# Performance work log

Measured on AMD Instinct MI355X. Metric: run time of the kernel, lower is better.

Reference implementation:

```python
import jax, jax.numpy as jnp
import numpy as np

N, IN_SIZE, FEAT, N_OUT = 8192, 512, 128, 512
ALPHA = 0.5


def setup_inputs() -> dict:
    key = jax.random.key(0)
    ks = jax.random.split(key, 5)
    return {
        "x": jax.random.normal(ks[0], (N, IN_SIZE), dtype=jnp.float32),
        "W0": jax.random.normal(ks[1], (FEAT, IN_SIZE), dtype=jnp.float32) * (1.0 / np.sqrt(IN_SIZE)),
        "W1": jax.random.normal(ks[2], (FEAT, IN_SIZE), dtype=jnp.float32) * (1.0 / np.sqrt(IN_SIZE)),
        "weight": jax.random.normal(ks[3], (IN_SIZE, N_OUT), dtype=jnp.float32),
        "weight_time": jax.random.normal(ks[4], (IN_SIZE, N_OUT), dtype=jnp.float32),
    }


def time_affinity(n: int) -> jnp.ndarray:
    # Closed form of the numpy roll/triu/flip construction: M[i,j] = n - |i-j|,
    # then rows normalized to sum to 1.
    idx = jnp.arange(n)
    M = (n - jnp.abs(idx[:, None] - idx[None, :])).astype(jnp.float32)
    return M / jnp.sum(M, axis=1, keepdims=True)


def reference(x, W0, W1, weight, weight_time):
    n = x.shape[0]
    q = x @ W0.T                      # [N, FEAT]
    k = x @ W1.T                      # [N, FEAT]
    G = jax.nn.softmax(q @ k.T, axis=1)   # [N, N] learned affinity
    G_time = time_affinity(n)              # [N, N] static affinity
    out = (G @ x) @ weight                 # [N, N_OUT]
    out_time = (G_time @ x) @ weight_time  # [N, N_OUT]
    return ALPHA * out + (1.0 - ALPHA) * out_time
```

## Files before the change

### kernel.cpp

```cpp
#include <hip/hip_runtime.h>
#include <math.h>

#define NN 8192
#define INS 512
#define FEAT 128

typedef unsigned short ush;
typedef short bf16x8 __attribute__((ext_vector_type(8)));
typedef float f32x4 __attribute__((ext_vector_type(4)));

__device__ __forceinline__ ush f2bf(float f) {
    unsigned u = __float_as_uint(f);
    unsigned r = (u + 0x7FFFu + ((u >> 16) & 1u)) >> 16;
    return (ush)r;
}
__device__ __forceinline__ float bf2f(ush h) {
    return __uint_as_float(((unsigned)h) << 16);
}
__device__ __forceinline__ void cp16(const ush* g, ush* l) {
    __builtin_amdgcn_global_load_lds(
        (const __attribute__((address_space(1))) void*)g,
        (__attribute__((address_space(3))) void*)l, 16, 0, 0);
}
__device__ __forceinline__ void split8(float4 f0, float4 f1, uint4& h, uint4& l) {
    float f[8] = {f0.x, f0.y, f0.z, f0.w, f1.x, f1.y, f1.z, f1.w};
    unsigned hu[8], lu[8];
    #pragma unroll
    for (int j = 0; j < 8; ++j) {
        unsigned u = __float_as_uint(f[j]);
        hu[j] = u >> 16;
        float lo = f[j] - __uint_as_float(u & 0xFFFF0000u);
        lu[j] = (unsigned)f2bf(lo);
    }
    h.x = hu[0] | (hu[1] << 16); h.y = hu[2] | (hu[3] << 16);
    h.z = hu[4] | (hu[5] << 16); h.w = hu[6] | (hu[7] << 16);
    l.x = lu[0] | (lu[1] << 16); l.y = lu[2] | (lu[3] << 16);
    l.z = lu[4] | (lu[5] << 16); l.w = lu[6] | (lu[7] << 16);
}


__global__ __launch_bounds__(256) void cast_w01(const float* __restrict__ W0,
                                                const float* __restrict__ W1,
                                                ush* __restrict__ W01h,
                                                ush* __restrict__ W01l) {
    int idx = (blockIdx.x * 256 + threadIdx.x) * 8;
    int r = idx >> 9, c = idx & 511;
    const float* src = (r < 128) ? &W0[r * 512 + c] : &W1[(r - 128) * 512 + c];
    float4 f0 = *(const float4*)src;
    float4 f1 = *(const float4*)(src + 4);
    uint4 h, l;
    split8(f0, f1, h, l);
    *(uint4*)&W01h[idx] = h;
    *(uint4*)&W01l[idx] = l;
}

__global__ __launch_bounds__(256) void cast_wT(const float* __restrict__ wm,
                                               const float* __restrict__ wt,
                                               ush* __restrict__ wmTh, ush* __restrict__ wmTl,
                                               ush* __restrict__ wtTh, ush* __restrict__ wtTl) {
    const float* src = blockIdx.z ? wt : wm;
    ush* oh = blockIdx.z ? wtTh : wmTh;
    ush* ol = blockIdx.z ? wtTl : wmTl;
    __shared__ float T[64][65];
    const int t = threadIdx.x;
    const int k0 = blockIdx.y * 64, n0 = blockIdx.x * 64;
    #pragma unroll
    for (int u = 0; u < 4; ++u) {
        int idx = u * 256 + t;
        int r = idx >> 4, c4 = (idx & 15) * 4;
        *(float4*)&T[r][c4] = *(const float4*)&src[(k0 + r) * 512 + n0 + c4];
    }
    __syncthreads();
    #pragma unroll
    for (int u = 0; u < 4; ++u) {
        int idx = u * 256 + t;
        int a = idx >> 4, b4 = (idx & 15) * 4;
        unsigned hu[4], lu[4];
        #pragma unroll
        for (int j = 0; j < 4; ++j) {
            float f = T[b4 + j][a];
            unsigned uu = __float_as_uint(f);
            hu[j] = uu >> 16;
            lu[j] = (unsigned)f2bf(f - __uint_as_float(uu & 0xFFFF0000u));
        }
        uint2 hp, lp;
        hp.x = hu[0] | (hu[1] << 16); hp.y = hu[2] | (hu[3] << 16);
        lp.x = lu[0] | (lu[1] << 16); lp.y = lu[2] | (lu[3] << 16);
        *(uint2*)&oh[(n0 + a) * 512 + k0 + b4] = hp;
        *(uint2*)&ol[(n0 + a) * 512 + k0 + b4] = lp;
    }
}

__global__ __launch_bounds__(256, 2) void gemm_xv(const float* __restrict__ x,
    const ush* __restrict__ wmTh, const ush* __restrict__ wmTl,
    const ush* __restrict__ wtTh, const ush* __restrict__ wtTl,
    ush* __restrict__ vtg, ush* __restrict__ xtb) {
    __shared__ __align__(16) ush smA[10240];
    __shared__ __align__(16) ush Bmh[2048], Bml[2048], Bth[2048], Btl[2048];
    ush* Ah = smA;
    ush* Al = smA + 5120;
    const int t = threadIdx.x;
    const int lane = t & 63, w = t >> 6;
    const int l15 = lane & 15, g4 = lane >> 4;
    const int m0 = blockIdx.y * 128, n0 = blockIdx.x * 64;
    const int wm0 = (w & 1) * 64, wn0 = (w >> 1) * 32;
    f32x4 accm[4][2], acct[4][2];
    #pragma unroll
    for (int mt = 0; mt < 4; ++mt)
        #pragma unroll
        for (int nt = 0; nt < 2; ++nt) {
            accm[mt][nt] = (f32x4){0.f, 0.f, 0.f, 0.f};
            acct[mt][nt] = (f32x4){0.f, 0.f, 0.f, 0.f};
        }

    const int am = t >> 1, akh = (t & 1) * 16;
    const int bn = t >> 2, bg = (t & 3) ^ ((t >> 2) & 3);
    for (int k0 = 0; k0 < 512; k0 += 32) {
        __syncthreads();
        {
            const float* src = &x[(m0 + am) * 512 + k0 + akh];
            float4 f0 = *(const float4*)&src[0];
            float4 f1 = *(const float4*)&src[4];
            float4 f2 = *(const float4*)&src[8];
            float4 f3 = *(const float4*)&src[12];
            uint4 h0, l0, h1, l1;
            split8(f0, f1, h0, l0);
            split8(f2, f3, h1, l1);
            int s0 = am * 5 + (akh >> 3);
            *(uint4*)&Ah[s0 * 8] = h0; *(uint4*)&Ah[(s0 + 1) * 8] = h1;
            *(uint4*)&Al[s0 * 8] = l0; *(uint4*)&Al[(s0 + 1) * 8] = l1;
        }
        {
            int srco = (n0 + bn) * 512 + k0 + bg * 8;
            cp16(&wmTh[srco], &Bmh[t * 8]);
            cp16(&wmTl[srco], &Bml[t * 8]);
            cp16(&wtTh[srco], &Bth[t * 8]);
            cp16(&wtTl[srco], &Btl[t * 8]);
        }
        __syncthreads();
        bf16x8 ah[4], al[4];
        #pragma unroll
        for (int mt = 0; mt < 4; ++mt) {
            int slot = (wm0 + mt * 16 + l15) * 5 + g4;
            ah[mt] = *(const bf16x8*)&Ah[slot * 8];
            al[mt] = *(const bf16x8*)&Al[slot * 8];
        }
        bf16x8 bmh[2], bml[2], bth[2], btl[2];
        #pragma unroll
        for (int nt = 0; nt < 2; ++nt) {
            int n = wn0 + nt * 16 + l15;
            int slot = n * 4 + (g4 ^ (n & 3));
            bmh[nt] = *(const bf16x8*)&Bmh[slot * 8];
            bml[nt] = *(const bf16x8*)&Bml[slot * 8];
            bth[nt] = *(const bf16x8*)&Bth[slot * 8];
            btl[nt] = *(const bf16x8*)&Btl[slot * 8];
        }
        #pragma unroll
        for (int mt = 0; mt < 4; ++mt)
            #pragma unroll
            for (int nt = 0; nt < 2; ++nt) {
                accm[mt][nt] = __builtin_amdgcn_mfma_f32_16x16x32_bf16(ah[mt], bmh[nt], accm[mt][nt], 0, 0, 0);
                accm[mt][nt] = __builtin_amdgcn_mfma_f32_16x16x32_bf16(al[mt], bmh[nt], accm[mt][nt], 0, 0, 0);
                accm[mt][nt] = __builtin_amdgcn_mfma_f32_16x16x32_bf16(ah[mt], bml[nt], accm[mt][nt], 0, 0, 0);
                acct[mt][nt] = __builtin_amdgcn_mfma_f32_16x16x32_bf16(ah[mt], bth[nt], acct[mt][nt], 0, 0, 0);
                acct[mt][nt] = __builtin_amdgcn_mfma_f32_16x16x32_bf16(al[mt], bth[nt], acct[mt][nt], 0, 0, 0);
                acct[mt][nt] = __builtin_amdgcn_mfma_f32_16x16x32_bf16(ah[mt], btl[nt], acct[mt][nt], 0, 0, 0);
            }
    }

    #pragma unroll
    for (int mt = 0; mt < 4; ++mt)
        #pragma unroll
        for (int nt = 0; nt < 2; ++nt) {
            int col = n0 + wn0 + nt * 16 + l15;
            int rowb = m0 + wm0 + mt * 16 + g4 * 4;
            #pragma unroll
            for (int reg = 0; reg < 4; ++reg)
                xtb[(rowb + reg) * 512 + col] = f2bf(acct[mt][nt][reg]);
        }
    __syncthreads();
    #pragma unroll
    for (int mt = 0; mt < 4; ++mt)
        #pragma unroll
        for (int nt = 0; nt < 2; ++nt) {
            int nl = wn0 + nt * 16 + l15;
            int mb = wm0 + mt * 16 + g4 * 4;
            uint2 pk;
            pk.x = (unsigned)f2bf(accm[mt][nt][0]) | ((unsigned)f2bf(accm[mt][nt][1]) << 16);
            pk.y = (unsigned)f2bf(accm[mt][nt][2]) | ((unsigned)f2bf(accm[mt][nt][3]) << 16);
            *(uint2*)&smA[nl * 136 + mb] = pk;
        }
    __syncthreads();
    {
        int a = t >> 2, off = (t & 3) * 32;
        #pragma unroll
        for (int u = 0; u < 4; ++u)
            *(uint4*)&vtg[(n0 + a) * 8192 + m0 + off + u * 8] =
                *(const uint4*)&smA[a * 136 + off + u * 8];
    }
}

__global__ __launch_bounds__(256) void gemm_qk(const float* __restrict__ x,
    const ush* __restrict__ W01h, const ush* __restrict__ W01l,
    ush* __restrict__ qh, ush* __restrict__ ql,
    ush* __restrict__ kh, ush* __restrict__ kl) {
    __shared__ __align__(16) ush sm[15360];
    ush* Ah = sm;
    ush* Al = sm + 2560;
    ush* Bh = sm + 5120;
    ush* Bl = sm + 10240;
    const int t = threadIdx.x;
    const int lane = t & 63, w = t >> 6;
    const int l15 = lane & 15, g4 = lane >> 4;
    const int m0 = blockIdx.y * 64, n0 = blockIdx.x * 128;
    const int wm0 = (w & 1) * 32, wn0 = (w >> 1) * 64;
    f32x4 acc[2][4];
    #pragma unroll
    for (int mt = 0; mt < 2; ++mt)
        #pragma unroll
        for (int nt = 0; nt < 4; ++nt)
            acc[mt][nt] = (f32x4){0.f, 0.f, 0.f, 0.f};

    const int ar = t >> 2, ag = t & 3;
    for (int k0 = 0; k0 < 512; k0 += 32) {
        __syncthreads();
        {
            const float* src = &x[(m0 + ar) * 512 + k0 + ag * 8];
            float4 f0 = *(const float4*)&src[0];
            float4 f1 = *(const float4*)&src[4];
            uint4 h, l;
            split8(f0, f1, h, l);
            int slot = ar * 5 + ag;
            *(uint4*)&Ah[slot * 8] = h;
            *(uint4*)&Al[slot * 8] = l;
        }
        #pragma unroll
        for (int u = 0; u < 2; ++u) {
            int s = u * 256 + t;
            int n = s >> 2, g = s & 3;
            int srco = (n0 + n) * 512 + k0 + g * 8;
            int slot = n * 5 + g;
            *(uint4*)&Bh[slot * 8] = *(const uint4*)&W01h[srco];
            *(uint4*)&Bl[slot * 8] = *(const uint4*)&W01l[srco];
        }
        __syncthreads();
        bf16x8 ah[2], al[2], bh[4], bl[4];
        #pragma unroll
        for (int mt = 0; mt < 2; ++mt) {
            int slot = (wm0 + mt * 16 + l15) * 5 + g4;
            ah[mt] = *(const bf16x8*)&Ah[slot * 8];
            al[mt] = *(const bf16x8*)&Al[slot * 8];
        }
        #pragma unroll
        for (int nt = 0; nt < 4; ++nt) {
            int slot = (wn0 + nt * 16 + l15) * 5 + g4;
            bh[nt] = *(const bf16x8*)&Bh[slot * 8];
            bl[nt] = *(const bf16x8*)&Bl[slot * 8];
        }
        #pragma unroll
        for (int mt = 0; mt < 2; ++mt)
            #pragma unroll
            for (int nt = 0; nt < 4; ++nt) {
                acc[mt][nt] = __builtin_amdgcn_mfma_f32_16x16x32_bf16(ah[mt], bh[nt], acc[mt][nt], 0, 0, 0);
                acc[mt][nt] = __builtin_amdgcn_mfma_f32_16x16x32_bf16(al[mt], bh[nt], acc[mt][nt], 0, 0, 0);
                acc[mt][nt] = __builtin_amdgcn_mfma_f32_16x16x32_bf16(ah[mt], bl[nt], acc[mt][nt], 0, 0, 0);
            }
    }
    ush* oh = (n0 == 0) ? qh : kh;
    ush* ol = (n0 == 0) ? ql : kl;
    #pragma unroll
    for (int mt = 0; mt < 2; ++mt)
        #pragma unroll
        for (int nt = 0; nt < 4; ++nt) {
            int col = wn0 + nt * 16 + l15;
            int rowb = m0 + wm0 + mt * 16 + g4 * 4;
            #pragma unroll
            for (int reg = 0; reg < 4; ++reg) {
                float v = acc[mt][nt][reg];
                unsigned u = __float_as_uint(v);
                ush h = (ush)(u >> 16);
                ush lo = f2bf(v - __uint_as_float(u & 0xFFFF0000u));
                oh[(rowb + reg) * 128 + col] = h;
                ol[(rowb + reg) * 128 + col] = lo;
            }
        }
}

__global__ __launch_bounds__(256) void time_part1(const ush* __restrict__ xtb,
                                                  float* __restrict__ pP,
                                                  float* __restrict__ pQ) {
    int d = blockIdx.x * 256 + threadIdx.x;
    int r0 = blockIdx.y * 128;
    float sp = 0.f, sq = 0.f;
    for (int r = 0; r < 128; ++r) {
        float v = bf2f(xtb[(r0 + r) * 512 + d]);
        sp += v;
        sq += (float)(r0 + r) * v;
    }
    pP[blockIdx.y * 512 + d] = sp;
    pQ[blockIdx.y * 512 + d] = sq;
}

__global__ __launch_bounds__(512) void time_part2(float* __restrict__ pP,
                                                  float* __restrict__ pQ,
                                                  float* __restrict__ Ad,
                                                  float* __restrict__ Qt) {
    int d = threadIdx.x;
    float rp = 0.f, rq = 0.f;
    for (int c = 0; c < 64; ++c) {
        int idx = c * 512 + d;
        float p = pP[idx], qv = pQ[idx];
        pP[idx] = rp; pQ[idx] = rq;
        rp += p; rq += qv;
    }
    Ad[d] = rp; Qt[d] = rq;
}

__global__ __launch_bounds__(256) void time_part3(const ush* __restrict__ xtb,
                                                  const float* __restrict__ pP,
                                                  const float* __restrict__ pQ,
                                                  const float* __restrict__ Ad,
                                                  const float* __restrict__ Qt,
                                                  float* __restrict__ out) {
    int d = blockIdx.x * 256 + threadIdx.x;
    int r0 = blockIdx.y * 128;
    float P = pP[blockIdx.y * 512 + d];
    float Q = pQ[blockIdx.y * 512 + d];
    float A = Ad[d], Qtot = Qt[d];
    for (int r = 0; r < 128; ++r) {
        int i = r0 + r;
        float v = bf2f(xtb[i * 512 + d]);
        P += v;
        float fi = (float)i;
        Q += fi * v;
        float B = 2.f * fi * P - 2.f * Q + Qtot - fi * A;
        int Si = 67108864 - (i * (i + 1)) / 2 - ((8191 - i) * (8192 - i)) / 2;
        float T = (8192.f * A - B) / (float)Si;
        out[i * 512 + d] = 0.5f * T;
    }
}

__global__ __launch_bounds__(512, 2) void pass2(const ush* __restrict__ qhg,
                                                const ush* __restrict__ qlg,
                                                const ush* __restrict__ khg,
                                                const ush* __restrict__ klg,
                                                const ush* __restrict__ vtg,
                                                ush* __restrict__ part0,
                                                ush* __restrict__ part1,
                                                float* __restrict__ lh) {
    __shared__ __align__(16) ush Kh0[512 * 8],  Kh1[512 * 8];
    __shared__ __align__(16) ush Kl0[512 * 8],  Kl1[512 * 8];
    __shared__ __align__(16) ush Vt0[2048 * 8], Vt1[2048 * 8];
    __shared__ __align__(16) ush Pd0[64 * 40],  Pd1[64 * 40];
    __shared__ float Linv[64];

    const int t = threadIdx.x;
    const int lane = t & 63, w = t >> 6;
    const int l15 = lane & 15, g = lane >> 4;
    const int b = blockIdx.x;
    const int xcd = b & 7, lid = b >> 3;
    const int jhalf = xcd >> 2;
    const int strip = (xcd & 3) * 32 + lid;
    const int i0 = strip * 64;
    const int jbase = jhalf * 4096;
    const bool isS = (w < 4);
    const int wp = w & 3;
    const float SHIFT = 32.0f;

    bf16x8 Qh[4], Ql[4];
    float l_run[4];
    if (isS) {
        int qrow = i0 + wp * 16 + l15;
        #pragma unroll
        for (int kt = 0; kt < 4; ++kt) {
            Qh[kt] = *(const bf16x8*)&qhg[qrow * 128 + kt * 32 + g * 8];
            Ql[kt] = *(const bf16x8*)&qlg[qrow * 128 + kt * 32 + g * 8];
        }
        #pragma unroll
        for (int reg = 0; reg < 4; ++reg) l_run[reg] = 0.f;
    }

    f32x4 acc[8][4];
    #pragma unroll
    for (int mt = 0; mt < 8; ++mt)
        #pragma unroll
        for (int nt = 0; nt < 4; ++nt)
            acc[mt][nt] = (f32x4){0.f, 0.f, 0.f, 0.f};

    auto stageK = [&](ush* KhD, ush* KlD, int j0) {
        int n = t >> 4, gl = (t & 15) ^ (n & 15);
        int src = (j0 + n) * 128 + gl * 8;
        cp16(&khg[src], &KhD[t * 8]);
        cp16(&klg[src], &KlD[t * 8]);
    };
    auto stageV = [&](ush* VtD, int j0) {
        #pragma unroll
        for (int u = 0; u < 4; ++u) {
            int s = u * 512 + t;
            int c = s >> 2, gl = (s & 3) ^ ((c >> 1) & 3);
            cp16(&vtg[c * 8192 + j0 + gl * 8], &VtD[s * 8]);
        }
    };
    auto pvStep = [&](const ush* VtR, const ush* Pr) {
        bf16x8 Pb[4];
        #pragma unroll
        for (int nt = 0; nt < 4; ++nt)
            Pb[nt] = *(const bf16x8*)&Pr[(nt * 16 + l15) * 40 + g * 8];
        #pragma unroll
        for (int mt = 0; mt < 8; ++mt) {
            int c = wp * 128 + mt * 16 + l15;
            int slot = c * 4 + (g ^ ((c >> 1) & 3));
            bf16x8 vfr = *(const bf16x8*)&VtR[slot * 8];
            #pragma unroll
            for (int nt = 0; nt < 4; ++nt)
                acc[mt][nt] = __builtin_amdgcn_mfma_f32_16x16x32_bf16(vfr, Pb[nt], acc[mt][nt], 0, 0, 0);
        }
    };

    stageK(Kh0, Kl0, jbase);
    __syncthreads();

    for (int jt = 0; jt < 128; ++jt) {
        ush* KhC = (jt & 1) ? Kh1 : Kh0;
        ush* KlC = (jt & 1) ? Kl1 : Kl0;
        ush* KhN = (jt & 1) ? Kh0 : Kh1;
        ush* KlN = (jt & 1) ? Kl0 : Kl1;
        ush* VtW = (jt & 1) ? Vt1 : Vt0;
        ush* VtR = (jt & 1) ? Vt0 : Vt1;
        ush* Pw  = (jt & 1) ? Pd1 : Pd0;
        ush* Pr  = (jt & 1) ? Pd0 : Pd1;

        stageV(VtW, jbase + jt * 32);
        if (jt < 127) stageK(KhN, KlN, jbase + (jt + 1) * 32);

        if (isS) {
            #pragma unroll
            for (int kh = 0; kh < 2; ++kh) {
                bf16x8 kbh[4], kbl[4];
                int n = kh * 16 + l15;
                #pragma unroll
                for (int kt = 0; kt < 4; ++kt) {
                    int slot = n * 16 + ((kt * 4 + g) ^ (n & 15));
                    kbh[kt] = *(const bf16x8*)&KhC[slot * 8];
                    kbl[kt] = *(const bf16x8*)&KlC[slot * 8];
                }
                f32x4 sa = {0.f, 0.f, 0.f, 0.f};
                f32x4 sb = {0.f, 0.f, 0.f, 0.f};
                f32x4 sc = {0.f, 0.f, 0.f, 0.f};
                #pragma unroll
                for (int kt = 0; kt < 4; ++kt) sa = __builtin_amdgcn_mfma_f32_16x16x32_bf16(Qh[kt], kbh[kt], sa, 0, 0, 0);
                #pragma unroll
                for (int kt = 0; kt < 4; ++kt) sb = __builtin_amdgcn_mfma_f32_16x16x32_bf16(Ql[kt], kbh[kt], sb, 0, 0, 0);
                #pragma unroll
                for (int kt = 0; kt < 4; ++kt) sc = __builtin_amdgcn_mfma_f32_16x16x32_bf16(Qh[kt], kbl[kt], sc, 0, 0, 0);
                #pragma unroll
                for (int reg = 0; reg < 4; ++reg) {
                    float s = (sa[reg] + sb[reg]) + sc[reg];
                    float p = __expf(s - SHIFT);
                    Pw[(wp * 16 + g * 4 + reg) * 40 + kh * 16 + l15] = f2bf(p);
                    l_run[reg] += p;
                }
            }
        } else if (jt > 0) {
            pvStep(VtR, Pr);
        }
        __syncthreads();
    }

    if (isS) {
        #pragma unroll
        for (int reg = 0; reg < 4; ++reg) {
            float rs = l_run[reg];
            #pragma unroll
            for (int st = 1; st < 16; st <<= 1) rs += __shfl_xor(rs, st);
            int row = wp * 16 + g * 4 + reg;
            if (l15 == 0) {
                Linv[row] = 1.0f / rs;
                lh[jhalf * 8192 + i0 + row] = rs;
            }
        }
    }
    __syncthreads();
    if (!isS) {
        pvStep(Vt1, Pd1);
        float li[4];
        #pragma unroll
        for (int nt = 0; nt < 4; ++nt) li[nt] = Linv[nt * 16 + l15];
        ush* prt = (jhalf == 0) ? part0 : part1;
        #pragma unroll
        for (int mt = 0; mt < 8; ++mt)
            #pragma unroll
            for (int nt = 0; nt < 4; ++nt) {
                int qrow = i0 + nt * 16 + l15;
                int vcol = wp * 128 + mt * 16 + g * 4;
                uint2 pk;
                pk.x = (unsigned)f2bf(acc[mt][nt][0] * li[nt]) |
                       ((unsigned)f2bf(acc[mt][nt][1] * li[nt]) << 16);
                pk.y = (unsigned)f2bf(acc[mt][nt][2] * li[nt]) |
                       ((unsigned)f2bf(acc[mt][nt][3] * li[nt]) << 16);
                *(uint2*)&prt[qrow * 512 + vcol] = pk;
            }
    }
}

__global__ __launch_bounds__(256) void merge_k(const ush* __restrict__ p0,
                                               const ush* __restrict__ p1,
                                               const float* __restrict__ lh,
                                               float* __restrict__ out) {
    int base = (blockIdx.x * 256 + threadIdx.x) * 8;
    int row = base >> 9;
    float l0 = lh[row], l1 = lh[8192 + row];
    float z = 0.5f / (l0 + l1);
    float w0 = l0 * z, w1 = l1 * z;
    uint4 a = *(const uint4*)&p0[base];
    uint4 b = *(const uint4*)&p1[base];
    float4 o0 = *(float4*)&out[base];
    float4 o1 = *(float4*)&out[base + 4];
    unsigned av[4] = {a.x, a.y, a.z, a.w};
    unsigned bv[4] = {b.x, b.y, b.z, b.w};
    float r[8];
    #pragma unroll
    for (int i = 0; i < 4; ++i) {
        r[2 * i + 0] = w0 * bf2f((ush)(av[i] & 0xFFFF)) + w1 * bf2f((ush)(bv[i] & 0xFFFF));
        r[2 * i + 1] = w0 * bf2f((ush)(av[i] >> 16))    + w1 * bf2f((ush)(bv[i] >> 16));
    }
    o0.x += r[0]; o0.y += r[1]; o0.z += r[2]; o0.w += r[3];
    o1.x += r[4]; o1.y += r[5]; o1.z += r[6]; o1.w += r[7];
    *(float4*)&out[base] = o0;
    *(float4*)&out[base + 4] = o1;
}

extern "C" void kernel_launch(void* const* d_in, const int* in_sizes, int n_in,
                              void* d_out, int out_size, void* d_ws, size_t ws_size,
                              hipStream_t stream) {
    const float* x  = (const float*)d_in[0];
    const float* W0 = (const float*)d_in[1];
    const float* W1 = (const float*)d_in[2];
    const float* wm = (const float*)d_in[3];
    const float* wt = (const float*)d_in[4];
    float* out = (float*)d_out;
    float* ws  = (float*)d_ws;

    ush* vtg = (ush*)(ws + 0);
    ush* xtb  = (ush*)(ws + 2097152);
    float* lhp = ws + 2097152;
    ush* W01h = (ush*)(ws + 4194304);
    ush* W01l = (ush*)(ws + 4259840);
    ush* wmTh = (ush*)(ws + 4325376);
    ush* wmTl = (ush*)(ws + 4456448);
    ush* wtTh = (ush*)(ws + 4587520);
    ush* wtTl = (ush*)(ws + 4718592);
    ush* part0 = (ush*)(ws + 4194304);
    ush* part1 = (ush*)(ws + 6291456);
    ush* qh = (ush*)(ws + 8388608);
    ush* ql = (ush*)(ws + 8912896);
    ush* kh = (ush*)(ws + 9437184);
    ush* kl = (ush*)(ws + 9961472);
    float* pP = ws + 10485760;
    float* pQ = ws + 10518528;
    float* Ad = ws + 10551296;
    float* Qt = ws + 10551808;

    cast_w01   <<<dim3(64),       256, 0, stream>>>(W0, W1, W01h, W01l);
    cast_wT    <<<dim3(8, 8, 2),  256, 0, stream>>>(wm, wt, wmTh, wmTl, wtTh, wtTl);
    gemm_xv    <<<dim3(8, 64),    256, 0, stream>>>(x, wmTh, wmTl, wtTh, wtTl, vtg, xtb);
    gemm_qk    <<<dim3(2, 128),   256, 0, stream>>>(x, W01h, W01l, qh, ql, kh, kl);
    time_part1 <<<dim3(2, 64),    256, 0, stream>>>(xtb, pP, pQ);
    time_part2 <<<dim3(1),        512, 0, stream>>>(pP, pQ, Ad, Qt);
    time_part3 <<<dim3(2, 64),    256, 0, stream>>>(xtb, pP, pQ, Ad, Qt, out);
    pass2      <<<dim3(256),      512, 0, stream>>>(qh, ql, kh, kl, vtg, part0, part1, lhp);
    merge_k    <<<dim3(2048),     256, 0, stream>>>(part0, part1, lhp, out);
}
```

Baseline: 312.5 us.

## Merge weight cast kernels, fold time scan into part3, retile qk GEMM

Merges the two weight-cast kernels into one launch and drops the single-block prefix-scan kernel by having each time_part3 block recompute its own prefix and totals from the partial sums. The qk projection GEMM is retiled so each block computes 32 rows against all 256 q/k columns. Its x tile is converted once per block, and the W tiles are loaded with direct global-to-LDS copies into an XOR-swizzled layout. The aim is fewer launches, less serialization and no reloading of the x tile across column blocks. In exchange every part3 block rereads all partial sums, and the qk grid shrinks to 256 blocks, each doing more work.

```diff
diff --git a/kernel.cpp b/kernel.cpp
--- a/kernel.cpp
+++ b/kernel.cpp
@@ -39,30 +39,32 @@
 }
 
 
-__global__ __launch_bounds__(256) void cast_w01(const float* __restrict__ W0,
+__global__ __launch_bounds__(256) void cast_all(const float* __restrict__ W0,
                                                 const float* __restrict__ W1,
+                                                const float* __restrict__ wm,
+                                                const float* __restrict__ wt,
                                                 ush* __restrict__ W01h,
-                                                ush* __restrict__ W01l) {
-    int idx = (blockIdx.x * 256 + threadIdx.x) * 8;
-    int r = idx >> 9, c = idx & 511;
-    const float* src = (r < 128) ? &W0[r * 512 + c] : &W1[(r - 128) * 512 + c];
-    float4 f0 = *(const float4*)src;
-    float4 f1 = *(const float4*)(src + 4);
-    uint4 h, l;
-    split8(f0, f1, h, l);
-    *(uint4*)&W01h[idx] = h;
-    *(uint4*)&W01l[idx] = l;
-}
-
-__global__ __launch_bounds__(256) void cast_wT(const float* __restrict__ wm,
-                                               const float* __restrict__ wt,
-                                               ush* __restrict__ wmTh, ush* __restrict__ wmTl,
-                                               ush* __restrict__ wtTh, ush* __restrict__ wtTl) {
+                                                ush* __restrict__ W01l,
+                                                ush* __restrict__ wmTh, ush* __restrict__ wmTl,
+                                                ush* __restrict__ wtTh, ush* __restrict__ wtTl) {
+    __shared__ float T[64][65];
+    const int t = threadIdx.x;
+    if (blockIdx.z == 2) {
+        int bid = blockIdx.y * 8 + blockIdx.x;
+        int idx = (bid * 256 + t) * 8;
+        int r = idx >> 9, c = idx & 511;
+        const float* src = (r < 128) ? &W0[r * 512 + c] : &W1[(r - 128) * 512 + c];
+        float4 f0 = *(const float4*)src;
+        float4 f1 = *(const float4*)(src + 4);
+        uint4 h, l;
+        split8(f0, f1, h, l);
+        *(uint4*)&W01h[idx] = h;
+        *(uint4*)&W01l[idx] = l;
+        return;
+    }
     const float* src = blockIdx.z ? wt : wm;
     ush* oh = blockIdx.z ? wtTh : wmTh;
     ush* ol = blockIdx.z ? wtTl : wmTl;
-    __shared__ float T[64][65];
-    const int t = threadIdx.x;
     const int k0 = blockIdx.y * 64, n0 = blockIdx.x * 64;
     #pragma unroll
     for (int u = 0; u < 4; ++u) {
@@ -200,31 +202,25 @@
     }
 }
 
-__global__ __launch_bounds__(256) void gemm_qk(const float* __restrict__ x,
+__global__ __launch_bounds__(256, 2) void gemm_qk(const float* __restrict__ x,
     const ush* __restrict__ W01h, const ush* __restrict__ W01l,
     ush* __restrict__ qh, ush* __restrict__ ql,
     ush* __restrict__ kh, ush* __restrict__ kl) {
-    __shared__ __align__(16) ush sm[15360];
-    ush* Ah = sm;
-    ush* Al = sm + 2560;
-    ush* Bh = sm + 5120;
-    ush* Bl = sm + 10240;
+    __shared__ __align__(16) ush Ah[1280], Al[1280];
+    __shared__ __align__(16) ush Bh[8192], Bl[8192];
     const int t = threadIdx.x;
     const int lane = t & 63, w = t >> 6;
     const int l15 = lane & 15, g4 = lane >> 4;
-    const int m0 = blockIdx.y * 64, n0 = blockIdx.x * 128;
-    const int wm0 = (w & 1) * 32, wn0 = (w >> 1) * 64;
-    f32x4 acc[2][4];
-    #pragma unroll
-    for (int mt = 0; mt < 2; ++mt)
-        #pragma unroll
-        for (int nt = 0; nt < 4; ++nt)
-            acc[mt][nt] = (f32x4){0.f, 0.f, 0.f, 0.f};
-
-    const int ar = t >> 2, ag = t & 3;
+    const int m0 = blockIdx.x * 32;
+    const int rw = w & 1, cw = w >> 1;
+    f32x4 acc[8];
+    #pragma unroll
+    for (int nt = 0; nt < 8; ++nt) acc[nt] = (f32x4){0.f, 0.f, 0.f, 0.f};
+
+    const int ar = (t & 127) >> 2, ag = t & 3;
     for (int k0 = 0; k0 < 512; k0 += 32) {
         __syncthreads();
-        {
+        if (t < 128) {
             const float* src = &x[(m0 + ar) * 512 + k0 + ag * 8];
             float4 f0 = *(const float4*)&src[0];
             float4 f1 = *(const float4*)&src[4];
@@ -235,55 +231,51 @@
             *(uint4*)&Al[slot * 8] = l;
         }
         #pragma unroll
-        for (int u = 0; u < 2; ++u) {
+        for (int u = 0; u < 4; ++u) {
             int s = u * 256 + t;
-            int n = s >> 2, g = s & 3;
-            int srco = (n0 + n) * 512 + k0 + g * 8;
-            int slot = n * 5 + g;
-            *(uint4*)&Bh[slot * 8] = *(const uint4*)&W01h[srco];
-            *(uint4*)&Bl[slot * 8] = *(const uint4*)&W01l[srco];
+            int n = s >> 2, gl = (s & 3) ^ (n & 3);
+            int srco = n * 512 + k0 + gl * 8;
+            cp16(&W01h[srco], &Bh[s * 8]);
+            cp16(&W01l[srco], &Bl[s * 8]);
         }
         __syncthreads();
-        bf16x8 ah[2], al[2], bh[4], bl[4];
-        #pragma unroll
-        for (int mt = 0; mt < 2; ++mt) {
-            int slot = (wm0 + mt * 16 + l15) * 5 + g4;
-            ah[mt] = *(const bf16x8*)&Ah[slot * 8];
-            al[mt] = *(const bf16x8*)&Al[slot * 8];
-        }
-        #pragma unroll
-        for (int nt = 0; nt < 4; ++nt) {
-            int slot = (wn0 + nt * 16 + l15) * 5 + g4;
+        bf16x8 ah, al;
+        {
+            int slot = (rw * 16 + l15) * 5 + g4;
+            ah = *(const bf16x8*)&Ah[slot * 8];
+            al = *(const bf16x8*)&Al[slot * 8];
+        }
+        bf16x8 bh[8], bl[8];
+        #pragma unroll
+        for (int nt = 0; nt < 8; ++nt) {
+            int n = cw * 128 + nt * 16 + l15;
+            int slot = n * 4 + (g4 ^ (n & 3));
             bh[nt] = *(const bf16x8*)&Bh[slot * 8];
             bl[nt] = *(const bf16x8*)&Bl[slot * 8];
         }
         #pragma unroll
-        for (int mt = 0; mt < 2; ++mt)
-            #pragma unroll
-            for (int nt = 0; nt < 4; ++nt) {
-                acc[mt][nt] = __builtin_amdgcn_mfma_f32_16x16x32_bf16(ah[mt], bh[nt], acc[mt][nt], 0, 0, 0);
-                acc[mt][nt] = __builtin_amdgcn_mfma_f32_16x16x32_bf16(al[mt], bh[nt], acc[mt][nt], 0, 0, 0);
-                acc[mt][nt] = __builtin_amdgcn_mfma_f32_16x16x32_bf16(ah[mt], bl[nt], acc[mt][nt], 0, 0, 0);
-            }
-    }
-    ush* oh = (n0 == 0) ? qh : kh;
-    ush* ol = (n0 == 0) ? ql : kl;
-    #pragma unroll
-    for (int mt = 0; mt < 2; ++mt)
-        #pragma unroll
-        for (int nt = 0; nt < 4; ++nt) {
-            int col = wn0 + nt * 16 + l15;
-            int rowb = m0 + wm0 + mt * 16 + g4 * 4;
-            #pragma unroll
-            for (int reg = 0; reg < 4; ++reg) {
-                float v = acc[mt][nt][reg];
-                unsigned u = __float_as_uint(v);
-                ush h = (ush)(u >> 16);
-                ush lo = f2bf(v - __uint_as_float(u & 0xFFFF0000u));
-                oh[(rowb + reg) * 128 + col] = h;
-                ol[(rowb + reg) * 128 + col] = lo;
-            }
-        }
+        for (int nt = 0; nt < 8; ++nt) {
+            acc[nt] = __builtin_amdgcn_mfma_f32_16x16x32_bf16(ah, bh[nt], acc[nt], 0, 0, 0);
+            acc[nt] = __builtin_amdgcn_mfma_f32_16x16x32_bf16(al, bh[nt], acc[nt], 0, 0, 0);
+            acc[nt] = __builtin_amdgcn_mfma_f32_16x16x32_bf16(ah, bl[nt], acc[nt], 0, 0, 0);
+        }
+    }
+    ush* oh = cw ? kh : qh;
+    ush* ol = cw ? kl : ql;
+    #pragma unroll
+    for (int nt = 0; nt < 8; ++nt) {
+        int col = nt * 16 + l15;
+        int rowb = m0 + rw * 16 + g4 * 4;
+        #pragma unroll
+        for (int reg = 0; reg < 4; ++reg) {
+            float v = acc[nt][reg];
+            unsigned u = __float_as_uint(v);
+            ush h = (ush)(u >> 16);
+            ush lo = f2bf(v - __uint_as_float(u & 0xFFFF0000u));
+            oh[(rowb + reg) * 128 + col] = h;
+            ol[(rowb + reg) * 128 + col] = lo;
+        }
+    }
 }
 
 __global__ __launch_bounds__(256) void time_part1(const ush* __restrict__ xtb,
@@ -301,32 +293,19 @@
     pQ[blockIdx.y * 512 + d] = sq;
 }
 
-__global__ __launch_bounds__(512) void time_part2(float* __restrict__ pP,
-                                                  float* __restrict__ pQ,
-                                                  float* __restrict__ Ad,
-                                                  float* __restrict__ Qt) {
-    int d = threadIdx.x;
-    float rp = 0.f, rq = 0.f;
-    for (int c = 0; c < 64; ++c) {
-        int idx = c * 512 + d;
-        float p = pP[idx], qv = pQ[idx];
-        pP[idx] = rp; pQ[idx] = rq;
-        rp += p; rq += qv;
-    }
-    Ad[d] = rp; Qt[d] = rq;
-}
-
 __global__ __launch_bounds__(256) void time_part3(const ush* __restrict__ xtb,
                                                   const float* __restrict__ pP,
                                                   const float* __restrict__ pQ,
-                                                  const float* __restrict__ Ad,
-                                                  const float* __restrict__ Qt,
                                                   float* __restrict__ out) {
     int d = blockIdx.x * 256 + threadIdx.x;
-    int r0 = blockIdx.y * 128;
-    float P = pP[blockIdx.y * 512 + d];
-    float Q = pQ[blockIdx.y * 512 + d];
-    float A = Ad[d], Qtot = Qt[d];
+    int y = blockIdx.y;
+    int r0 = y * 128;
+    float P = 0.f, Q = 0.f, A = 0.f, Qtot = 0.f;
+    for (int c = 0; c < 64; ++c) {
+        if (c == y) { P = A; Q = Qtot; }
+        A += pP[c * 512 + d];
+        Qtot += pQ[c * 512 + d];
+    }
     for (int r = 0; r < 128; ++r) {
         int i = r0 + r;
         float v = bf2f(xtb[i * 512 + d]);
@@ -558,16 +537,12 @@
     ush* kl = (ush*)(ws + 9961472);
     float* pP = ws + 10485760;
     float* pQ = ws + 10518528;
-    float* Ad = ws + 10551296;
-    float* Qt = ws + 10551808;
-
-    cast_w01   <<<dim3(64),       256, 0, stream>>>(W0, W1, W01h, W01l);
-    cast_wT    <<<dim3(8, 8, 2),  256, 0, stream>>>(wm, wt, wmTh, wmTl, wtTh, wtTl);
+
+    cast_all   <<<dim3(8, 8, 3),  256, 0, stream>>>(W0, W1, wm, wt, W01h, W01l, wmTh, wmTl, wtTh, wtTl);
     gemm_xv    <<<dim3(8, 64),    256, 0, stream>>>(x, wmTh, wmTl, wtTh, wtTl, vtg, xtb);
-    gemm_qk    <<<dim3(2, 128),   256, 0, stream>>>(x, W01h, W01l, qh, ql, kh, kl);
+    gemm_qk    <<<dim3(256),      256, 0, stream>>>(x, W01h, W01l, qh, ql, kh, kl);
     time_part1 <<<dim3(2, 64),    256, 0, stream>>>(xtb, pP, pQ);
-    time_part2 <<<dim3(1),        512, 0, stream>>>(pP, pQ, Ad, Qt);
-    time_part3 <<<dim3(2, 64),    256, 0, stream>>>(xtb, pP, pQ, Ad, Qt, out);
+    time_part3 <<<dim3(2, 64),    256, 0, stream>>>(xtb, pP, pQ, out);
     pass2      <<<dim3(256),      512, 0, stream>>>(qh, ql, kh, kl, vtg, part0, part1, lhp);
     merge_k    <<<dim3(2048),     256, 0, stream>>>(part0, part1, lhp, out);
 }
```

Result: no change. 312.4 us (-0.0%).
